# Kernel optimization log

Measured on AMD Instinct MI355X. Metric: run time of the kernel, lower is better.

The kernel has to match this reference:

```python
import jax, jax.numpy as jnp
import numpy as np

LAT = (4, 24, 24, 24, 24, 3, 3)  # [mu, L0, L1, L2, L3, 3, 3]


def setup_inputs() -> dict:
    key = jax.random.key(0)
    k1, k2 = jax.random.split(key)
    U_re = jax.random.normal(k1, LAT, dtype=jnp.float32)
    U_im = jax.random.normal(k2, LAT, dtype=jnp.float32)
    return {"U_re": U_re, "U_im": U_im}


def _polyakov_dir(Umu, axis, L):
    """P(x) = prod_{k=0}^{L-1} U_mu(x + k*mu_hat) via a sequential scan of
    batched 3x3 complex matmuls. Umu: [L0,L1,L2,L3,3,3] complex."""

    def step(carry, _):
        P, Ush = carry
        Ush = jnp.roll(Ush, -1, axis=axis)  # U_mu(x + (k)*mu_hat)
        P = jnp.einsum('...ij,...jk->...ik', P, Ush)
        return (P, Ush), None

    (P, _), _ = jax.lax.scan(step, (Umu, Umu), None, length=L - 1)
    return P


def reference(U_re, U_im):
    U = jax.lax.complex(U_re, U_im)  # complex64 link field
    loops = jnp.stack([
        _polyakov_dir(U[mu], mu, U.shape[1 + mu]) for mu in range(4)
    ])  # [4, L0, L1, L2, L3, 3, 3] complex
    # return real/imag stacked so output is a real array
    return jnp.stack([loops.real, loops.imag])
```

## Files before the change

### kernel.cpp

```cpp
#include <hip/hip_runtime.h>

#define LSIZE 24
#define VOL (LSIZE*LSIZE*LSIZE*LSIZE)
#define NLINES (LSIZE*LSIZE*LSIZE)
#define LPB 8
#define TPB 64
#define IMG 1728
#define NCHUNK 864

__device__ __forceinline__ void cmul(const float* __restrict__ ar, const float* __restrict__ ai,
                                     const float* __restrict__ br, const float* __restrict__ bi,
                                     float* __restrict__ or_, float* __restrict__ oi_) {
#pragma unroll
  for (int i = 0; i < 3; ++i) {
#pragma unroll
    for (int j = 0; j < 3; ++j) {
      float sr = 0.f, si = 0.f;
#pragma unroll
      for (int m = 0; m < 3; ++m) {
        float x = ar[i*3+m], y = ai[i*3+m];
        float u = br[m*3+j], v = bi[m*3+j];
        sr = fmaf(x, u, sr);
        sr = fmaf(-y, v, sr);
        si = fmaf(x, v, si);
        si = fmaf(y, u, si);
      }
      or_[i*3+j] = sr;
      oi_[i*3+j] = si;
    }
  }
}

__device__ __forceinline__ void cp9(float* dr, float* di, const float* sr, const float* si) {
#pragma unroll
  for (int e = 0; e < 9; ++e) { dr[e] = sr[e]; di[e] = si[e]; }
}

__device__ __forceinline__ void setid(float* r, float* im) {
#pragma unroll
  for (int e = 0; e < 9; ++e) { r[e] = (e == 0 || e == 4 || e == 8) ? 1.f : 0.f; im[e] = 0.f; }
}

__device__ __forceinline__ void shup(float* dr, float* di, const float* sr, const float* si, int delta) {
#pragma unroll
  for (int e = 0; e < 9; ++e) {
    dr[e] = __shfl_up(sr[e], (unsigned)delta, 64);
    di[e] = __shfl_up(si[e], (unsigned)delta, 64);
  }
}
__device__ __forceinline__ void shdn(float* dr, float* di, const float* sr, const float* si, int delta) {
#pragma unroll
  for (int e = 0; e < 9; ++e) {
    dr[e] = __shfl_down(sr[e], (unsigned)delta, 64);
    di[e] = __shfl_down(si[e], (unsigned)delta, 64);
  }
}

__device__ __forceinline__ void ldm9(const float* __restrict__ L, float* v) {
#pragma unroll
  for (int e = 0; e < 9; ++e) v[e] = L[e];
}
__device__ __forceinline__ void stm9(float* __restrict__ L, const float* v) {
#pragma unroll
  for (int e = 0; e < 9; ++e) L[e] = v[e];
}

__global__ __launch_bounds__(TPB, 3) void polyakov_1w(
    const float* __restrict__ U_re, const float* __restrict__ U_im,
    float* __restrict__ out) {
  __shared__ __align__(16) float lds[2 * IMG];

  const int lane = threadIdx.x;
  const int bid  = blockIdx.x;
  const int mu   = bid / (NLINES / LPB);
  const int l0   = (bid - mu * (NLINES / LPB)) * LPB;

  const int cC0 = l0 % LSIZE;
  const int cB0 = (l0 / LSIZE) % LSIZE;
  const int cA0 = l0 / (LSIZE * LSIZE);

  int s00, st;
  if (mu == 0)      { s00 = l0;                                st = 13824; }
  else if (mu == 1) { s00 = cA0*13824 + cB0*24  + cC0;         st = 576;   }
  else if (mu == 2) { s00 = cA0*13824 + cB0*576 + cC0;         st = 24;    }
  else              { s00 = l0 * 24;                           st = 1;     }

  const float* __restrict__ gR = U_re + (size_t)mu * (VOL*9);
  const float* __restrict__ gI = U_im + (size_t)mu * (VOL*9);

#pragma unroll
  for (int p = 0; p < 14; ++p) {
    int c = p * 64 + lane;
    if (c < NCHUNK) {
      int d   = c << 2;
      int arr = d >= IMG;
      int da  = d - (arr ? IMG : 0);
      int g;
      if (mu == 3) g = s00 * 9 + da;
      else { int slab = da / 72; g = (s00 + slab * st) * 9 + (da - slab * 72); }
      const float* src = (arr ? gI : gR) + g;
      __builtin_amdgcn_global_load_lds(
          (const __attribute__((address_space(1))) void*)(const void*)src,
          (__attribute__((address_space(3))) void*)(void*)(lds + p * 256),
          16, 0, 0);
    }
  }
  asm volatile("s_waitcnt vmcnt(0)" ::: "memory");
  __builtin_amdgcn_sched_barrier(0);

  const int tl = lane >> 3;
  const int ll = lane & 7;
  const int k0 = 3 * tl;
  const int uo = (mu == 3) ? ll * 216 : ll * 9;
  const int ks = (mu == 3) ? 9 : 72;
  float* mR = lds + uo;
  float* mI = lds + IMG + uo;

  float Br[9], Bi[9], Yr[9], Yi[9], Tr[9], Ti[9];
  {
    float Ar[9], Ai[9];
    ldm9(mR + (k0+0)*ks, Yr); ldm9(mI + (k0+0)*ks, Yi);
    ldm9(mR + (k0+1)*ks, Ar); ldm9(mI + (k0+1)*ks, Ai);
    cmul(Yr, Yi, Ar, Ai, Tr, Ti);
    ldm9(mR + (k0+2)*ks, Ar); ldm9(mI + (k0+2)*ks, Ai);
    cmul(Tr, Ti, Ar, Ai, Br, Bi);
  }

  float Pr[9], Pi[9];
  {
    float Xr[9], Xi[9];
    cp9(Xr, Xi, Br, Bi);
#pragma unroll
    for (int d = 1; d < 8; d <<= 1) {
      shup(Yr, Yi, Xr, Xi, 8 * d);
      if (tl >= d) { cmul(Yr, Yi, Xr, Xi, Tr, Ti); cp9(Xr, Xi, Tr, Ti); }
    }
    shup(Pr, Pi, Xr, Xi, 8);
    if (tl == 0) setid(Pr, Pi);
  }
  float Rr[9], Ri[9];
  {
    float Zr[9], Zi[9];
    cp9(Zr, Zi, Br, Bi);
#pragma unroll
    for (int d = 1; d < 8; d <<= 1) {
      shdn(Yr, Yi, Zr, Zi, 8 * d);
      if (tl + d < 8) { cmul(Zr, Zi, Yr, Yi, Tr, Ti); cp9(Zr, Zi, Tr, Ti); }
    }
    shdn(Yr, Yi, Zr, Zi, 8);
    if (tl == 7) setid(Yr, Yi);
    cmul(Yr, Yi, Pr, Pi, Rr, Ri);
  }

  ldm9(mR + (k0+0)*ks, Pr); ldm9(mI + (k0+0)*ks, Pi);
  cmul(Br, Bi, Rr, Ri, Tr, Ti);
  stm9(mR + (k0+0)*ks, Tr); stm9(mI + (k0+0)*ks, Ti);

  float W2r[9], W2i[9], U1r[9], U1i[9], W1r[9], W1i[9];
  ldm9(mR + (k0+2)*ks, Yr); ldm9(mI + (k0+2)*ks, Yi);
  cmul(Yr, Yi, Rr, Ri, W2r, W2i);
  ldm9(mR + (k0+1)*ks, U1r); ldm9(mI + (k0+1)*ks, U1i);
  cmul(U1r, U1i, W2r, W2i, W1r, W1i);
  cmul(W1r, W1i, Pr, Pi, Tr, Ti);
  stm9(mR + (k0+1)*ks, Tr); stm9(mI + (k0+1)*ks, Ti);
  cmul(W2r, W2i, Pr, Pi, Yr, Yi);
  cmul(Yr, Yi, U1r, U1i, Tr, Ti);
  stm9(mR + (k0+2)*ks, Tr); stm9(mI + (k0+2)*ks, Ti);

  asm volatile("s_waitcnt lgkmcnt(0)" ::: "memory");
  __builtin_amdgcn_sched_barrier(0);

  float* __restrict__ oR = out + (size_t)mu * (VOL*9);
  float* __restrict__ oI = out + (size_t)(4 + mu) * (VOL*9);
#pragma unroll
  for (int p = 0; p < 14; ++p) {
    int c = p * 64 + lane;
    if (c < NCHUNK) {
      int d   = c << 2;
      int arr = d >= IMG;
      int da  = d - (arr ? IMG : 0);
      int g;
      if (mu == 3) g = s00 * 9 + da;
      else { int slab = da / 72; g = (s00 + slab * st) * 9 + (da - slab * 72); }
      float4 v = *(const float4*)(lds + d);
      *(float4*)((arr ? oI : oR) + g) = v;
    }
  }
}

extern "C" void kernel_launch(void* const* d_in, const int* in_sizes, int n_in,
                              void* d_out, int out_size, void* d_ws, size_t ws_size,
                              hipStream_t stream) {
  const float* U_re = (const float*)d_in[0];
  const float* U_im = (const float*)d_in[1];
  float* out = (float*)d_out;
  int nblocks = 4 * NLINES / LPB;
  hipLaunchKernelGGL(polyakov_1w, dim3(nblocks), dim3(TPB), 0, stream, U_re, U_im, out);
}
```

Before: 178.5 us.

## Process two tiles per block and prefetch the next tile through registers

Each block now handles two consecutive line-octets instead of one. It prefetches the next tile's link data into a 14-entry float4 register stage while the current tile is computed in LDS. The direct global-to-LDS loads are replaced by ordinary global loads followed by LDS stores, and only half as many blocks are launched. The aim is to hide global load latency behind the matrix-product compute, at the cost of extra VGPR pressure and fewer blocks in flight.

```diff
diff --git a/kernel.cpp b/kernel.cpp
--- a/kernel.cpp
+++ b/kernel.cpp
@@ -5,6 +5,8 @@
 #define NLINES (LSIZE*LSIZE*LSIZE)
 #define LPB 8
 #define TPB 64
+#define NT 2
+#define OCT (NLINES/LPB)
 #define IMG 1728
 #define NCHUNK 864
 
@@ -65,125 +67,162 @@
   for (int e = 0; e < 9; ++e) L[e] = v[e];
 }
 
-__global__ __launch_bounds__(TPB, 3) void polyakov_1w(
+struct Tile { int mu, s00, st; };
+
+__device__ __forceinline__ Tile tileGeom(int O) {
+  Tile tg;
+  int mu = O / OCT;
+  int l0 = (O - mu * OCT) * LPB;
+  int cC0 = l0 % LSIZE;
+  int cB0 = (l0 / LSIZE) % LSIZE;
+  int cA0 = l0 / (LSIZE * LSIZE);
+  if (mu == 0)      { tg.s00 = l0;                          tg.st = 13824; }
+  else if (mu == 1) { tg.s00 = cA0*13824 + cB0*24 + cC0;    tg.st = 576; }
+  else if (mu == 2) { tg.s00 = cA0*13824 + cB0*576 + cC0;   tg.st = 24; }
+  else              { tg.s00 = l0 * 24;                     tg.st = 1; }
+  tg.mu = mu;
+  return tg;
+}
+
+__device__ __forceinline__ int chunkAddr(int mu, int s00, int st, int da) {
+  if (mu == 3) return s00 * 9 + da;
+  int slab = da / 72;
+  return (s00 + slab * st) * 9 + (da - slab * 72);
+}
+
+__global__ __launch_bounds__(TPB, 3) void polyakov_pipe(
     const float* __restrict__ U_re, const float* __restrict__ U_im,
     float* __restrict__ out) {
   __shared__ __align__(16) float lds[2 * IMG];
 
   const int lane = threadIdx.x;
-  const int bid  = blockIdx.x;
-  const int mu   = bid / (NLINES / LPB);
-  const int l0   = (bid - mu * (NLINES / LPB)) * LPB;
-
-  const int cC0 = l0 % LSIZE;
-  const int cB0 = (l0 / LSIZE) % LSIZE;
-  const int cA0 = l0 / (LSIZE * LSIZE);
-
-  int s00, st;
-  if (mu == 0)      { s00 = l0;                                st = 13824; }
-  else if (mu == 1) { s00 = cA0*13824 + cB0*24  + cC0;         st = 576;   }
-  else if (mu == 2) { s00 = cA0*13824 + cB0*576 + cC0;         st = 24;    }
-  else              { s00 = l0 * 24;                           st = 1;     }
-
-  const float* __restrict__ gR = U_re + (size_t)mu * (VOL*9);
-  const float* __restrict__ gI = U_im + (size_t)mu * (VOL*9);
-
-#pragma unroll
-  for (int p = 0; p < 14; ++p) {
-    int c = p * 64 + lane;
-    if (c < NCHUNK) {
-      int d   = c << 2;
-      int arr = d >= IMG;
-      int da  = d - (arr ? IMG : 0);
-      int g;
-      if (mu == 3) g = s00 * 9 + da;
-      else { int slab = da / 72; g = (s00 + slab * st) * 9 + (da - slab * 72); }
-      const float* src = (arr ? gI : gR) + g;
-      __builtin_amdgcn_global_load_lds(
-          (const __attribute__((address_space(1))) void*)(const void*)src,
-          (__attribute__((address_space(3))) void*)(void*)(lds + p * 256),
-          16, 0, 0);
-    }
-  }
-  asm volatile("s_waitcnt vmcnt(0)" ::: "memory");
-  __builtin_amdgcn_sched_barrier(0);
-
-  const int tl = lane >> 3;
-  const int ll = lane & 7;
-  const int k0 = 3 * tl;
-  const int uo = (mu == 3) ? ll * 216 : ll * 9;
-  const int ks = (mu == 3) ? 9 : 72;
-  float* mR = lds + uo;
-  float* mI = lds + IMG + uo;
-
-  float Br[9], Bi[9], Yr[9], Yi[9], Tr[9], Ti[9];
+  float4 stg[14];
+
   {
-    float Ar[9], Ai[9];
-    ldm9(mR + (k0+0)*ks, Yr); ldm9(mI + (k0+0)*ks, Yi);
-    ldm9(mR + (k0+1)*ks, Ar); ldm9(mI + (k0+1)*ks, Ai);
-    cmul(Yr, Yi, Ar, Ai, Tr, Ti);
-    ldm9(mR + (k0+2)*ks, Ar); ldm9(mI + (k0+2)*ks, Ai);
-    cmul(Tr, Ti, Ar, Ai, Br, Bi);
-  }
-
-  float Pr[9], Pi[9];
-  {
-    float Xr[9], Xi[9];
-    cp9(Xr, Xi, Br, Bi);
-#pragma unroll
-    for (int d = 1; d < 8; d <<= 1) {
-      shup(Yr, Yi, Xr, Xi, 8 * d);
-      if (tl >= d) { cmul(Yr, Yi, Xr, Xi, Tr, Ti); cp9(Xr, Xi, Tr, Ti); }
-    }
-    shup(Pr, Pi, Xr, Xi, 8);
-    if (tl == 0) setid(Pr, Pi);
-  }
-  float Rr[9], Ri[9];
-  {
-    float Zr[9], Zi[9];
-    cp9(Zr, Zi, Br, Bi);
-#pragma unroll
-    for (int d = 1; d < 8; d <<= 1) {
-      shdn(Yr, Yi, Zr, Zi, 8 * d);
-      if (tl + d < 8) { cmul(Zr, Zi, Yr, Yi, Tr, Ti); cp9(Zr, Zi, Tr, Ti); }
-    }
-    shdn(Yr, Yi, Zr, Zi, 8);
-    if (tl == 7) setid(Yr, Yi);
-    cmul(Yr, Yi, Pr, Pi, Rr, Ri);
-  }
-
-  ldm9(mR + (k0+0)*ks, Pr); ldm9(mI + (k0+0)*ks, Pi);
-  cmul(Br, Bi, Rr, Ri, Tr, Ti);
-  stm9(mR + (k0+0)*ks, Tr); stm9(mI + (k0+0)*ks, Ti);
-
-  float W2r[9], W2i[9], U1r[9], U1i[9], W1r[9], W1i[9];
-  ldm9(mR + (k0+2)*ks, Yr); ldm9(mI + (k0+2)*ks, Yi);
-  cmul(Yr, Yi, Rr, Ri, W2r, W2i);
-  ldm9(mR + (k0+1)*ks, U1r); ldm9(mI + (k0+1)*ks, U1i);
-  cmul(U1r, U1i, W2r, W2i, W1r, W1i);
-  cmul(W1r, W1i, Pr, Pi, Tr, Ti);
-  stm9(mR + (k0+1)*ks, Tr); stm9(mI + (k0+1)*ks, Ti);
-  cmul(W2r, W2i, Pr, Pi, Yr, Yi);
-  cmul(Yr, Yi, U1r, U1i, Tr, Ti);
-  stm9(mR + (k0+2)*ks, Tr); stm9(mI + (k0+2)*ks, Ti);
-
-  asm volatile("s_waitcnt lgkmcnt(0)" ::: "memory");
-  __builtin_amdgcn_sched_barrier(0);
-
-  float* __restrict__ oR = out + (size_t)mu * (VOL*9);
-  float* __restrict__ oI = out + (size_t)(4 + mu) * (VOL*9);
-#pragma unroll
-  for (int p = 0; p < 14; ++p) {
-    int c = p * 64 + lane;
-    if (c < NCHUNK) {
-      int d   = c << 2;
-      int arr = d >= IMG;
-      int da  = d - (arr ? IMG : 0);
-      int g;
-      if (mu == 3) g = s00 * 9 + da;
-      else { int slab = da / 72; g = (s00 + slab * st) * 9 + (da - slab * 72); }
-      float4 v = *(const float4*)(lds + d);
-      *(float4*)((arr ? oI : oR) + g) = v;
+    Tile tg = tileGeom(blockIdx.x * NT);
+    const float* __restrict__ gR = U_re + (size_t)tg.mu * (VOL*9);
+    const float* __restrict__ gI = U_im + (size_t)tg.mu * (VOL*9);
+#pragma unroll
+    for (int p = 0; p < 14; ++p) {
+      int c = p * 64 + lane;
+      if (c < NCHUNK) {
+        int d = c << 2;
+        int arr = d >= IMG;
+        int da = d - (arr ? IMG : 0);
+        stg[p] = *(const float4*)((arr ? gI : gR) + chunkAddr(tg.mu, tg.s00, tg.st, da));
+      }
+    }
+  }
+
+#pragma unroll 1
+  for (int t = 0; t < NT; ++t) {
+    const Tile tg = tileGeom(blockIdx.x * NT + t);
+    const int mu = tg.mu;
+
+    if (t == 0) { asm volatile("s_waitcnt vmcnt(0)" ::: "memory"); }
+    else        { asm volatile("s_waitcnt vmcnt(14)" ::: "memory"); }
+    asm volatile("s_waitcnt lgkmcnt(0)" ::: "memory");
+    __builtin_amdgcn_sched_barrier(0);
+
+#pragma unroll
+    for (int p = 0; p < 14; ++p) {
+      int c = p * 64 + lane;
+      if (c < NCHUNK) *(float4*)(&lds[c << 2]) = stg[p];
+    }
+
+    if (t + 1 < NT) {
+      Tile tn = tileGeom(blockIdx.x * NT + t + 1);
+      const float* __restrict__ gR = U_re + (size_t)tn.mu * (VOL*9);
+      const float* __restrict__ gI = U_im + (size_t)tn.mu * (VOL*9);
+#pragma unroll
+      for (int p = 0; p < 14; ++p) {
+        int c = p * 64 + lane;
+        if (c < NCHUNK) {
+          int d = c << 2;
+          int arr = d >= IMG;
+          int da = d - (arr ? IMG : 0);
+          stg[p] = *(const float4*)((arr ? gI : gR) + chunkAddr(tn.mu, tn.s00, tn.st, da));
+        }
+      }
+    }
+
+    asm volatile("s_waitcnt lgkmcnt(0)" ::: "memory");
+    __builtin_amdgcn_sched_barrier(0);
+
+    const int tl = lane >> 3;
+    const int ll = lane & 7;
+    const int k0 = 3 * tl;
+    const int uo = (mu == 3) ? ll * 216 : ll * 9;
+    const int ks = (mu == 3) ? 9 : 72;
+    float* mR = lds + uo;
+    float* mI = lds + IMG + uo;
+
+    float Br[9], Bi[9], Yr[9], Yi[9], Tr[9], Ti[9];
+    {
+      float Ar[9], Ai[9];
+      ldm9(mR + (k0+0)*ks, Yr); ldm9(mI + (k0+0)*ks, Yi);
+      ldm9(mR + (k0+1)*ks, Ar); ldm9(mI + (k0+1)*ks, Ai);
+      cmul(Yr, Yi, Ar, Ai, Tr, Ti);
+      ldm9(mR + (k0+2)*ks, Ar); ldm9(mI + (k0+2)*ks, Ai);
+      cmul(Tr, Ti, Ar, Ai, Br, Bi);
+    }
+
+    float Pr[9], Pi[9];
+    {
+      float Xr[9], Xi[9];
+      cp9(Xr, Xi, Br, Bi);
+#pragma unroll
+      for (int d = 1; d < 8; d <<= 1) {
+        shup(Yr, Yi, Xr, Xi, 8 * d);
+        if (tl >= d) { cmul(Yr, Yi, Xr, Xi, Tr, Ti); cp9(Xr, Xi, Tr, Ti); }
+      }
+      shup(Pr, Pi, Xr, Xi, 8);
+      if (tl == 0) setid(Pr, Pi);
+    }
+    float Rr[9], Ri[9];
+    {
+      float Zr[9], Zi[9];
+      cp9(Zr, Zi, Br, Bi);
+#pragma unroll
+      for (int d = 1; d < 8; d <<= 1) {
+        shdn(Yr, Yi, Zr, Zi, 8 * d);
+        if (tl + d < 8) { cmul(Zr, Zi, Yr, Yi, Tr, Ti); cp9(Zr, Zi, Tr, Ti); }
+      }
+      shdn(Yr, Yi, Zr, Zi, 8);
+      if (tl == 7) setid(Yr, Yi);
+      cmul(Yr, Yi, Pr, Pi, Rr, Ri);
+    }
+
+    ldm9(mR + (k0+0)*ks, Pr); ldm9(mI + (k0+0)*ks, Pi);
+    cmul(Br, Bi, Rr, Ri, Tr, Ti);
+    stm9(mR + (k0+0)*ks, Tr); stm9(mI + (k0+0)*ks, Ti);
+
+    float W2r[9], W2i[9], U1r[9], U1i[9], W1r[9], W1i[9];
+    ldm9(mR + (k0+2)*ks, Yr); ldm9(mI + (k0+2)*ks, Yi);
+    cmul(Yr, Yi, Rr, Ri, W2r, W2i);
+    ldm9(mR + (k0+1)*ks, U1r); ldm9(mI + (k0+1)*ks, U1i);
+    cmul(U1r, U1i, W2r, W2i, W1r, W1i);
+    cmul(W1r, W1i, Pr, Pi, Tr, Ti);
+    stm9(mR + (k0+1)*ks, Tr); stm9(mI + (k0+1)*ks, Ti);
+    cmul(W2r, W2i, Pr, Pi, Yr, Yi);
+    cmul(Yr, Yi, U1r, U1i, Tr, Ti);
+    stm9(mR + (k0+2)*ks, Tr); stm9(mI + (k0+2)*ks, Ti);
+
+    asm volatile("s_waitcnt lgkmcnt(0)" ::: "memory");
+    __builtin_amdgcn_sched_barrier(0);
+
+    float* __restrict__ oR = out + (size_t)mu * (VOL*9);
+    float* __restrict__ oI = out + (size_t)(4 + mu) * (VOL*9);
+#pragma unroll
+    for (int p = 0; p < 14; ++p) {
+      int c = p * 64 + lane;
+      if (c < NCHUNK) {
+        int d = c << 2;
+        int arr = d >= IMG;
+        int da = d - (arr ? IMG : 0);
+        float4 v = *(const float4*)(&lds[d]);
+        *(float4*)((arr ? oI : oR) + chunkAddr(mu, tg.s00, tg.st, da)) = v;
+      }
     }
   }
 }
@@ -194,6 +233,6 @@
   const float* U_re = (const float*)d_in[0];
   const float* U_im = (const float*)d_in[1];
   float* out = (float*)d_out;
-  int nblocks = 4 * NLINES / LPB;
-  hipLaunchKernelGGL(polyakov_1w, dim3(nblocks), dim3(TPB), 0, stream, U_re, U_im, out);
-}
+  int nblocks = 4 * OCT / NT;
+  hipLaunchKernelGGL(polyakov_pipe, dim3(nblocks), dim3(TPB), 0, stream, U_re, U_im, out);
+}
```

Result: slower. 284.0 us (+59.1%).
